# Kernel optimization log

Measured on AMD Instinct MI355X. Metric: run time of the kernel, lower is better.

## Reference

```python
import jax, jax.numpy as jnp
import numpy as np

D_MODEL, D_HEAD, N_HEADS, D_LATENT, D_ROPE = 2048, 128, 16, 512, 64
ROPE_BASE = 10000.0
SCALE = 1.0 / np.sqrt(D_HEAD + D_ROPE)


def _rope(x):
    # x: [B, H, T, d_rope]; GPT-NeoX style half-split rotary
    T, d = x.shape[-2], x.shape[-1]
    inv_freq = 1.0 / (ROPE_BASE ** (jnp.arange(0, d, 2, dtype=jnp.float32) / d))
    ang = jnp.arange(T, dtype=jnp.float32)[:, None] * inv_freq[None, :]  # [T, d/2]
    cos = jnp.concatenate([jnp.cos(ang), jnp.cos(ang)], axis=-1)  # [T, d]
    sin = jnp.concatenate([jnp.sin(ang), jnp.sin(ang)], axis=-1)
    x1, x2 = x[..., : d // 2], x[..., d // 2 :]
    rot = jnp.concatenate([-x2, x1], axis=-1)
    return x * cos + rot * sin


def setup_inputs() -> dict:
    key = jax.random.key(0)
    ks = jax.random.split(key, 8)
    B, T = 2, 2048
    s = 0.02
    inp = {
        "x": jax.random.normal(ks[0], (B, T, D_MODEL), jnp.float32),
        "w_q": jax.random.normal(ks[1], (D_MODEL, D_MODEL), jnp.float32) * s,
        "w_dkv": jax.random.normal(ks[2], (D_LATENT, D_MODEL), jnp.float32) * s,
        "w_ukv": jax.random.normal(ks[3], (2 * D_MODEL, D_LATENT), jnp.float32) * s,
        "w_o": jax.random.normal(ks[4], (D_MODEL, D_MODEL), jnp.float32) * s,
        "w_q_rot": jax.random.normal(ks[5], (N_HEADS * D_ROPE, D_MODEL), jnp.float32) * s,
        "w_k_rot": jax.random.normal(ks[6], (D_ROPE, D_MODEL), jnp.float32) * s,
        "mask": jnp.triu(jnp.ones((T, T), dtype=bool), 1),  # True = blocked (causal)
    }
    return inp


def reference(x, w_q, w_dkv, w_ukv, w_o, w_q_rot, w_k_rot, mask):
    B, T, _ = x.shape
    # content queries  [B, H, T, d_head]
    q = (x @ w_q.T).reshape(B, T, N_HEADS, D_HEAD).transpose(0, 2, 1, 3)
    # latent KV compression -> expansion
    dkv = x @ w_dkv.T                       # [B, T, d_latent]
    ukv = (dkv @ w_ukv.T).reshape(B, T, N_HEADS, 2 * D_HEAD).transpose(0, 2, 1, 3)
    k, v = ukv[..., :D_HEAD], ukv[..., D_HEAD:]
    # decoupled rope parts
    q_rot = (x @ w_q_rot.T).reshape(B, T, N_HEADS, D_ROPE).transpose(0, 2, 1, 3)
    k_rot = jnp.broadcast_to((x @ w_k_rot.T)[:, None, :, :], (B, N_HEADS, T, D_ROPE))
    q = jnp.concatenate([q, _rope(q_rot)], axis=-1)   # [B, H, T, d_head+d_rope]
    k = jnp.concatenate([k, _rope(k_rot)], axis=-1)
    # SDPA with True-means-blocked mask
    scores = jnp.einsum("bhqd,bhkd->bhqk", q, k) * SCALE
    scores = jnp.where(mask, -jnp.inf, scores)
    attn = jax.nn.softmax(scores, axis=-1)
    out = jnp.einsum("bhqk,bhkd->bhqd", attn, v)      # [B, H, T, d_head]
    out = out.transpose(0, 2, 1, 3).reshape(B, T, D_MODEL)
    return out @ w_o.T
```

## Files before the change

kernel.cpp:

```cpp
#include <hip/hip_runtime.h>
#include <hip/hip_bf16.h>
#include <math.h>

#define T_SEQ 2048
#define QSTR  3648

typedef __bf16 bf16x8 __attribute__((ext_vector_type(8)));
typedef float  f32x4  __attribute__((ext_vector_type(4)));
typedef float  f32x16 __attribute__((ext_vector_type(16)));
typedef unsigned int u32x4 __attribute__((ext_vector_type(4)));

#define GLOAD_LDS16(g, l) __builtin_amdgcn_global_load_lds( \
    (const __attribute__((address_space(1))) void*)(g),      \
    (__attribute__((address_space(3))) void*)(l), 16, 0, 0)

#define VMCNT(n) asm volatile("s_waitcnt vmcnt(" #n ")" ::: "memory")

static __device__ __forceinline__ unsigned cvtpk_bf16(float a, float b)
{
    unsigned r;
    asm("v_cvt_pk_bf16_f32 %0, %1, %2" : "=v"(r) : "v"(a), "v"(b));
    return r;
}

__global__ __launch_bounds__(256) void cast_bf16(const float* __restrict__ src,
                                                 __bf16* __restrict__ dst, int n)
{
    int i = (blockIdx.x * 256 + threadIdx.x) * 8;
    if (i < n) {
        float4 a = *reinterpret_cast<const float4*>(src + i);
        float4 b = *reinterpret_cast<const float4*>(src + i + 4);
        bf16x8 f;
        f[0] = (__bf16)a.x; f[1] = (__bf16)a.y; f[2] = (__bf16)a.z; f[3] = (__bf16)a.w;
        f[4] = (__bf16)b.x; f[5] = (__bf16)b.y; f[6] = (__bf16)b.z; f[7] = (__bf16)b.w;
        *reinterpret_cast<bf16x8*>(dst + i) = f;
    }
}

__global__ __launch_bounds__(256) void rope_ip(__bf16* buf, int shift, int stride,
                                               int total)
{
    int gid = blockIdx.x * 256 + threadIdx.x;
    if (gid >= total) return;
    int row = gid >> shift;
    int rem = gid & ((1 << shift) - 1);
    int hb = rem >> 5, j = rem & 31;
    int t = row & (T_SEQ - 1);
    const float L2B = 0.4152410118609203f;
    float freq = exp2f(-L2B * (float)j);
    float sn, cs;
    __sincosf((float)t * freq, &sn, &cs);
    size_t base = (size_t)row * stride + hb * 64 + j;
    float v1 = (float)buf[base], v2 = (float)buf[base + 32];
    buf[base]      = (__bf16)(v1 * cs - v2 * sn);
    buf[base + 32] = (__bf16)(v2 * cs + v1 * sn);
}

__global__ __launch_bounds__(256) void prep_v(const __bf16* __restrict__ ukv,
                                              __bf16* __restrict__ vtt)
{
    __shared__ __align__(16) __bf16 Ls[64 * 136];
    const int tid = threadIdx.x;
    const int u = blockIdx.x, bh = blockIdx.y;
    const int b = bh >> 4, h = bh & 15;
    const size_t base = (size_t)b * T_SEQ + u * 64;
    #pragma unroll
    for (int p = 0; p < 4; p++) {
        int c = tid + 256 * p;
        int k = c >> 4, dv8 = (c & 15) * 8;
        *reinterpret_cast<bf16x8*>(Ls + k * 136 + dv8) =
            *reinterpret_cast<const bf16x8*>(ukv + (base + k) * 4096 + h * 256 + 128 + dv8);
    }
    __syncthreads();
    #pragma unroll
    for (int p = 0; p < 4; p++) {
        int c = tid + 256 * p;
        int dv = c >> 3, kb = c & 7;
        bf16x8 f;
        #pragma unroll
        for (int i = 0; i < 8; i++) f[i] = Ls[(kb * 8 + i) * 136 + dv];
        *reinterpret_cast<bf16x8*>(vtt + (((size_t)bh * 32 + u) * 128 + dv) * 64
                                   + ((kb ^ (dv & 7)) << 3)) = f;
    }
}

template <typename OutT>
__global__ __launch_bounds__(512) void gemm_bt_8ph(const __bf16* __restrict__ A,
                                                   int lda,
                                                   const __bf16* __restrict__ B,
                                                   OutT* __restrict__ C,
                                                   int M, int N, int K)
{
    __shared__ __align__(16) __bf16 S[2 * 24576];
    const int tid  = threadIdx.x;
    const int lane = tid & 63;
    const int w    = tid >> 6;
    const int l15  = lane & 15, quad = lane >> 4;
    const int wm = w >> 2, wn = w & 3;
    const int m0 = blockIdx.y * 128, n0 = blockIdx.x * 256;
    const int NT = K >> 6;

    f32x4 acc[4][4] = {};

    const int lrA = tid >> 3, segA = tid & 7;

    auto stageA = [&](int T1, int h) {
        int d = T1 & 1;
        int g = ((lrA >> 5) << 6) + h * 32 + (lrA & 31);
        GLOAD_LDS16(A + (size_t)(m0 + g) * lda + T1 * 64 + ((segA ^ (lrA & 7)) << 3),
                    S + d * 24576 + h * 4096 + tid * 8);
    };
    auto stageB = [&](int T1, int h) {
        int d = T1 & 1;
        #pragma unroll
        for (int i = 0; i < 2; i++) {
            int c = i * 512 + tid;
            int lr = c >> 3, seg = c & 7;
            int g = n0 + ((lr >> 5) << 6) + h * 32 + (lr & 31);
            if (g >= N) g = N - 1;
            GLOAD_LDS16(B + (size_t)g * K + T1 * 64 + ((seg ^ (lr & 7)) << 3),
                        S + d * 24576 + 8192 + h * 8192 + c * 8);
        }
    };

#define PHASE(d, mh, nh, STAGE, WAIT) do {                                     \
    const __bf16* Ah_ = S + (d) * 24576 + (mh) * 4096;                         \
    const __bf16* Bh_ = S + (d) * 24576 + 8192 + (nh) * 8192;                  \
    bf16x8 af[2][2], bfr[2][2];                                                \
    _Pragma("unroll")                                                          \
    for (int mr = 0; mr < 2; mr++) {                                           \
        int ar = wm * 32 + mr * 16 + l15;                                      \
        _Pragma("unroll")                                                      \
        for (int kk = 0; kk < 2; kk++)                                         \
            af[mr][kk] = *reinterpret_cast<const bf16x8*>(                     \
                Ah_ + ar * 64 + (((kk * 4 + quad) ^ (ar & 7)) << 3));          \
    }                                                                          \
    _Pragma("unroll")                                                          \
    for (int nr = 0; nr < 2; nr++) {                                           \
        int br = wn * 32 + nr * 16 + l15;                                      \
        _Pragma("unroll")                                                      \
        for (int kk = 0; kk < 2; kk++)                                         \
            bfr[nr][kk] = *reinterpret_cast<const bf16x8*>(                    \
                Bh_ + br * 64 + (((kk * 4 + quad) ^ (br & 7)) << 3));          \
    }                                                                          \
    STAGE;                                                                     \
    WAIT;                                                                      \
    __builtin_amdgcn_s_barrier();                                              \
    asm volatile("s_waitcnt lgkmcnt(0)" ::: "memory");                         \
    __builtin_amdgcn_sched_barrier(0);                                         \
    __builtin_amdgcn_s_setprio(1);                                             \
    _Pragma("unroll")                                                          \
    for (int mr = 0; mr < 2; mr++)                                             \
        _Pragma("unroll")                                                      \
        for (int nr = 0; nr < 2; nr++)                                         \
            _Pragma("unroll")                                                  \
            for (int kk = 0; kk < 2; kk++)                                     \
                acc[(mh) * 2 + mr][(nh) * 2 + nr] =                            \
                    __builtin_amdgcn_mfma_f32_16x16x32_bf16(                   \
                        af[mr][kk], bfr[nr][kk],                               \
                        acc[(mh) * 2 + mr][(nh) * 2 + nr], 0, 0, 0);           \
    __builtin_amdgcn_s_setprio(0);                                             \
} while (0)

    stageA(0, 0);
    stageB(0, 0);
    stageB(0, 1);
    stageA(0, 1);
    VMCNT(3);
    __builtin_amdgcn_s_barrier();

    for (int T = 0; T < NT - 1; T++) {
        const int d = T & 1;
        PHASE(d, 0, 0, stageA(T + 1, 0), VMCNT(2));
        PHASE(d, 0, 1, stageB(T + 1, 0), VMCNT(3));
        PHASE(d, 1, 0, stageB(T + 1, 1), (void)0);
        PHASE(d, 1, 1, stageA(T + 1, 1), VMCNT(3));
    }
    {
        const int d = (NT - 1) & 1;
        PHASE(d, 0, 0, (void)0, VMCNT(1));
        PHASE(d, 0, 1, (void)0, VMCNT(0));
        PHASE(d, 1, 0, (void)0, (void)0);
        PHASE(d, 1, 1, (void)0, (void)0);
    }
#undef PHASE

    #pragma unroll
    for (int ai = 0; ai < 4; ai++) {
        #pragma unroll
        for (int bj = 0; bj < 4; bj++) {
            int col = n0 + wn * 64 + bj * 16 + l15;
            if (col < N) {
                #pragma unroll
                for (int r = 0; r < 4; r++) {
                    size_t row = m0 + wm * 64 + ai * 16 + quad * 4 + r;
                    C[row * (size_t)N + col] = (OutT)acc[ai][bj][r];
                }
            }
        }
    }
}

__global__ __launch_bounds__(256, 2) void flash_mfma(
    const __bf16* __restrict__ qcat, const __bf16* __restrict__ ukv,
    const __bf16* __restrict__ vtt, __bf16* __restrict__ obuf)
{
    __shared__ __align__(16) __bf16 LDS[40960];

    const int tid  = threadIdx.x;
    const int w    = tid >> 6;
    const int lane = tid & 63;
    const int l31  = lane & 31;
    const int lh   = lane >> 5;
    const int l15  = lane & 15;
    const int quad = lane >> 4;
    const int gx = blockIdx.x, gy = blockIdx.y;
    int bh, qi;
    if (gy < 16) { bh = gy * 2;            qi = gx; }
    else         { bh = (gy - 16) * 2 + 1; qi = 15 - gx; }
    const int b = bh >> 4, h = bh & 15;
    const int q0 = qi * 128;
    const float SCALE = 0.07216878364870323f;
    const size_t urow = (size_t)b * T_SEQ;

    const int q = q0 + 32 * w + l31;
    bf16x8 qf[12];
    {
        const __bf16* qrow = qcat + (urow + q) * QSTR + h * 128;
        #pragma unroll
        for (int dk = 0; dk < 8; dk++)
            qf[dk] = *reinterpret_cast<const bf16x8*>(qrow + 16 * dk + 8 * lh);
        const __bf16* qrr = qcat + (urow + q) * QSTR + 2048 + h * 64;
        #pragma unroll
        for (int dk = 0; dk < 4; dk++)
            qf[8 + dk] = *reinterpret_cast<const bf16x8*>(qrr + 16 * dk + 8 * lh);
    }

    f32x16 o[4] = {};
    float m_i = -INFINITY, l_i = 0.f;

    const int nunits = 2 * qi + 2;

    auto stage = [&](int x) {
        const int d1 = x & 1;
        const size_t roff = urow + (size_t)64 * x;
        #pragma unroll
        for (int p = 0; p < 4; p++) {
            int c = tid + 256 * p;
            int row = c >> 4, seg = c & 15;
            GLOAD_LDS16(ukv + (roff + row) * 4096 + h * 256 + ((seg ^ (row & 7)) << 3),
                        LDS + d1 * 8192 + c * 8);
        }
        #pragma unroll
        for (int p = 0; p < 2; p++) {
            int c = tid + 256 * p;
            int row = c >> 3, seg = c & 7;
            GLOAD_LDS16(qcat + (roff + row) * QSTR + 3072 + ((seg ^ (row & 7)) << 3),
                        LDS + 16384 + d1 * 4096 + c * 8);
        }
        const __bf16* vsrc = vtt + ((size_t)bh * 32 + x) * 8192;
        #pragma unroll
        for (int p = 0; p < 4; p++) {
            int c = tid + 256 * p;
            GLOAD_LDS16(vsrc + c * 8, LDS + 24576 + d1 * 8192 + c * 8);
        }
    };

    stage(0);
    VMCNT(0);
    __builtin_amdgcn_s_barrier();

    for (int u = 0; u < nunits; u++) {
        if (u + 1 < nunits) { stage(u + 1); VMCNT(10); }
        else                { VMCNT(0); }
        __builtin_amdgcn_s_barrier();
        __builtin_amdgcn_sched_barrier(0);

        const int d1 = u & 1;
        const __bf16* KN = LDS + d1 * 8192;
        const __bf16* KR = LDS + 16384 + d1 * 4096;
        const __bf16* VT = LDS + 24576 + d1 * 8192;
        const int key = l31 & 7;

        f32x16 s2[2] = {};
        __builtin_amdgcn_s_setprio(1);
        #pragma unroll
        for (int t = 0; t < 2; t++) {
            const __bf16* kn = KN + (32 * t + l31) * 128;
            const __bf16* kr = KR + (32 * t + l31) * 64;
            #pragma unroll
            for (int dk = 0; dk < 8; dk++) {
                bf16x8 kf = *reinterpret_cast<const bf16x8*>(kn + (((2 * dk + lh) ^ key) << 3));
                s2[t] = __builtin_amdgcn_mfma_f32_32x32x16_bf16(kf, qf[dk], s2[t], 0, 0, 0);
            }
            #pragma unroll
            for (int dk = 0; dk < 4; dk++) {
                bf16x8 kf = *reinterpret_cast<const bf16x8*>(kr + (((2 * dk + lh) ^ key) << 3));
                s2[t] = __builtin_amdgcn_mfma_f32_32x32x16_bf16(kf, qf[8 + dk], s2[t], 0, 0, 0);
            }
        }
        __builtin_amdgcn_s_setprio(0);

        const int k0 = 64 * u;
        const bool domask = (u + 2 >= nunits);
        float rmax = -INFINITY;
        #pragma unroll
        for (int t = 0; t < 2; t++)
            #pragma unroll
            for (int g = 0; g < 16; g++) {
                float v = s2[t][g] * SCALE;
                if (domask) {
                    int kg = k0 + 32 * t + (g & 3) + 8 * (g >> 2) + 4 * lh;
                    if (kg > q) v = -INFINITY;
                }
                s2[t][g] = v;
                rmax = fmaxf(rmax, v);
            }
        rmax = fmaxf(rmax, __shfl_xor(rmax, 32, 64));
        const float mnew  = fmaxf(m_i, rmax);
        const float alpha = __expf(m_i - mnew);
        m_i = mnew;
        float part = 0.f;
        #pragma unroll
        for (int t = 0; t < 2; t++)
            #pragma unroll
            for (int g = 0; g < 16; g++) {
                float pv = __expf(s2[t][g] - mnew);
                s2[t][g] = pv;
                part += pv;
            }
        l_i = l_i * alpha + part;
        #pragma unroll
        for (int dt = 0; dt < 4; dt++) o[dt] *= alpha;

        __builtin_amdgcn_s_setprio(1);
        #pragma unroll
        for (int t = 0; t < 2; t++) {
            unsigned Ap[4], Bp[4];
            #pragma unroll
            for (int g = 0; g < 4; g++) {
                Ap[g] = cvtpk_bf16(s2[t][4 * g],     s2[t][4 * g + 1]);
                Bp[g] = cvtpk_bf16(s2[t][4 * g + 2], s2[t][4 * g + 3]);
            }
            #pragma unroll
            for (int sub = 0; sub < 2; sub++) {
                unsigned xA = lh ? Ap[2 * sub] : Ap[2 * sub + 1];
                unsigned xB = lh ? Bp[2 * sub] : Bp[2 * sub + 1];
                unsigned rA = __shfl_xor(xA, 32, 64);
                unsigned rB = __shfl_xor(xB, 32, 64);
                u32x4 uv;
                uv[0] = lh ? rA : Ap[2 * sub];
                uv[1] = lh ? rB : Bp[2 * sub];
                uv[2] = lh ? Ap[2 * sub + 1] : rA;
                uv[3] = lh ? Bp[2 * sub + 1] : rB;
                bf16x8 pf = __builtin_bit_cast(bf16x8, uv);
                const int s = 2 * t + sub;
                #pragma unroll
                for (int dt = 0; dt < 4; dt++) {
                    bf16x8 vf = *reinterpret_cast<const bf16x8*>(
                        VT + (32 * dt + l31) * 64 + (((2 * s + lh) ^ key) << 3));
                    o[dt] = __builtin_amdgcn_mfma_f32_32x32x16_bf16(vf, pf, o[dt], 0, 0, 0);
                }
            }
        }
        __builtin_amdgcn_s_setprio(0);

        __builtin_amdgcn_sched_barrier(0);
        __builtin_amdgcn_s_barrier();
    }

    const float linv = 1.0f / (l_i + __shfl_xor(l_i, 32, 64));
    float* Os = reinterpret_cast<float*>(LDS);
    #pragma unroll
    for (int dt = 0; dt < 4; dt++)
        #pragma unroll
        for (int g = 0; g < 16; g++) {
            int d = 32 * dt + (g & 3) + 8 * (g >> 2) + 4 * lh;
            Os[(32 * w + l31) * 132 + d] = o[dt][g] * linv;
        }
    asm volatile("s_waitcnt lgkmcnt(0)" ::: "memory");
    __builtin_amdgcn_sched_barrier(0);
    #pragma unroll
    for (int p = 0; p < 8; p++) {
        int row = 32 * w + 4 * p + quad;
        float4 a  = *reinterpret_cast<const float4*>(Os + row * 132 + 8 * l15);
        float4 c2 = *reinterpret_cast<const float4*>(Os + row * 132 + 8 * l15 + 4);
        bf16x8 f;
        f[0] = (__bf16)a.x;  f[1] = (__bf16)a.y;  f[2] = (__bf16)a.z;  f[3] = (__bf16)a.w;
        f[4] = (__bf16)c2.x; f[5] = (__bf16)c2.y; f[6] = (__bf16)c2.z; f[7] = (__bf16)c2.w;
        *reinterpret_cast<bf16x8*>(obuf + (urow + q0 + row) * 2048 + h * 128 + 8 * l15) = f;
    }
}

extern "C" void kernel_launch(void* const* d_in, const int* in_sizes, int n_in,
                              void* d_out, int out_size, void* d_ws, size_t ws_size,
                              hipStream_t stream)
{
    const float* x      = (const float*)d_in[0];
    const float* w_q    = (const float*)d_in[1];
    const float* w_dkv  = (const float*)d_in[2];
    const float* w_ukv  = (const float*)d_in[3];
    const float* w_o    = (const float*)d_in[4];
    const float* w_qrot = (const float*)d_in[5];
    const float* w_krot = (const float*)d_in[6];
    float* out = (float*)d_out;

    const size_t M = 4096;
    __bf16* ws   = (__bf16*)d_ws;
    __bf16* xb   = ws;
    __bf16* wcat = xb + M * 2048;
    __bf16* wqb  = wcat;
    __bf16* wqrb = wcat + (size_t)2048 * 2048;
    __bf16* wkrb = wqrb + (size_t)1024 * 2048;
    __bf16* wdkb = wkrb + (size_t)64 * 2048;
    __bf16* wukb = wcat + (size_t)QSTR * 2048;
    __bf16* wob  = wukb + (size_t)4096 * 512;
    __bf16* qcat = wob  + (size_t)2048 * 2048;
    __bf16* ukv  = qcat + M * QSTR;
    __bf16* ao   = ukv  + M * 4096;
    __bf16* vtt  = ao   + M * 2048;

    dim3 blk(256);
    cast_bf16<<<4096, blk, 0, stream>>>(x,      xb,   4096 * 2048);
    cast_bf16<<<2048, blk, 0, stream>>>(w_q,    wqb,  2048 * 2048);
    cast_bf16<<<1024, blk, 0, stream>>>(w_qrot, wqrb, 1024 * 2048);
    cast_bf16<<<64,   blk, 0, stream>>>(w_krot, wkrb, 64 * 2048);
    cast_bf16<<<512,  blk, 0, stream>>>(w_dkv,  wdkb, 512 * 2048);
    cast_bf16<<<1024, blk, 0, stream>>>(w_ukv,  wukb, 4096 * 512);
    cast_bf16<<<2048, blk, 0, stream>>>(w_o,    wob,  2048 * 2048);

    gemm_bt_8ph<__bf16><<<dim3(15, 32), dim3(512), 0, stream>>>(
        xb, 2048, wcat, qcat, 4096, QSTR, 2048);
    gemm_bt_8ph<__bf16><<<dim3(16, 32), dim3(512), 0, stream>>>(
        qcat + 3136, QSTR, wukb, ukv, 4096, 4096, 512);

    rope_ip<<<8192, blk, 0, stream>>>(qcat + 2048, 9, QSTR, 4096 * 512);
    rope_ip<<<512,  blk, 0, stream>>>(qcat + 3072, 5, QSTR, 4096 * 32);
    prep_v<<<dim3(32, 32), blk, 0, stream>>>(ukv, vtt);

    flash_mfma<<<dim3(16, 32), blk, 0, stream>>>(qcat, ukv, vtt, ao);

    gemm_bt_8ph<float><<<dim3(8, 32), dim3(512), 0, stream>>>(
        ao, 2048, wob, out, 4096, 2048, 2048);
}
```

Baseline: 394.6 us.

## Merge weight casts into one launch and use 256x256 GEMM tiles for projections

The seven separate fp32-to-bf16 cast launches become one kernel that picks its source and destination from a cumulative block-offset table. The two projection GEMMs move from 128x256 to 256x256 tiles using a new four-phase pipelined kernel with 128 KB of shared memory and 32 accumulators per thread. Larger tiles raise arithmetic intensity and halve global reloads of the weight operand. The cost is fewer blocks (240 and 256) on a GPU with many CUs, plus higher register and LDS pressure.

```diff
diff --git a/kernel.cpp b/kernel.cpp
--- a/kernel.cpp
+++ b/kernel.cpp
@@ -23,18 +23,28 @@
     return r;
 }
 
-__global__ __launch_bounds__(256) void cast_bf16(const float* __restrict__ src,
-                                                 __bf16* __restrict__ dst, int n)
-{
-    int i = (blockIdx.x * 256 + threadIdx.x) * 8;
-    if (i < n) {
-        float4 a = *reinterpret_cast<const float4*>(src + i);
-        float4 b = *reinterpret_cast<const float4*>(src + i + 4);
-        bf16x8 f;
-        f[0] = (__bf16)a.x; f[1] = (__bf16)a.y; f[2] = (__bf16)a.z; f[3] = (__bf16)a.w;
-        f[4] = (__bf16)b.x; f[5] = (__bf16)b.y; f[6] = (__bf16)b.z; f[7] = (__bf16)b.w;
-        *reinterpret_cast<bf16x8*>(dst + i) = f;
-    }
+struct CastArgs {
+    const float* s[7];
+    __bf16*      d[7];
+    unsigned     cum[8];
+};
+
+__global__ __launch_bounds__(256) void cast_all(CastArgs a)
+{
+    const unsigned blk = blockIdx.x;
+    int idx = 0;
+    #pragma unroll
+    for (int i = 1; i < 7; i++) if (blk >= a.cum[i]) idx = i;
+    const unsigned local = blk - a.cum[idx];
+    const float* src = a.s[idx];
+    __bf16* dst = a.d[idx];
+    const int i = (int)(local * 256 + threadIdx.x) * 8;
+    float4 va = *reinterpret_cast<const float4*>(src + i);
+    float4 vb = *reinterpret_cast<const float4*>(src + i + 4);
+    bf16x8 f;
+    f[0] = (__bf16)va.x; f[1] = (__bf16)va.y; f[2] = (__bf16)va.z; f[3] = (__bf16)va.w;
+    f[4] = (__bf16)vb.x; f[5] = (__bf16)vb.y; f[6] = (__bf16)vb.z; f[7] = (__bf16)vb.w;
+    *reinterpret_cast<bf16x8*>(dst + i) = f;
 }
 
 __global__ __launch_bounds__(256) void rope_ip(__bf16* buf, int shift, int stride,
@@ -81,6 +91,133 @@
         for (int i = 0; i < 8; i++) f[i] = Ls[(kb * 8 + i) * 136 + dv];
         *reinterpret_cast<bf16x8*>(vtt + (((size_t)bh * 32 + u) * 128 + dv) * 64
                                    + ((kb ^ (dv & 7)) << 3)) = f;
+    }
+}
+
+template <typename OutT>
+__global__ __launch_bounds__(512, 2) void gemm_bt_256(const __bf16* __restrict__ A,
+                                                      int lda,
+                                                      const __bf16* __restrict__ B,
+                                                      OutT* __restrict__ C,
+                                                      int M, int N, int K)
+{
+    __shared__ __align__(16) __bf16 S[2 * 32768];
+    const int tid  = threadIdx.x;
+    const int lane = tid & 63;
+    const int w    = tid >> 6;
+    const int l15  = lane & 15, quad = lane >> 4;
+    const int wm = w >> 2, wn = w & 3;
+    const int m0 = blockIdx.y * 256, n0 = blockIdx.x * 256;
+    const int NT = K >> 6;
+
+    f32x4 acc[8][4] = {};
+    bf16x8 af[4][2], bfr[2][2];
+
+    auto stageA = [&](int T1, int h) {
+        int d = T1 & 1;
+        #pragma unroll
+        for (int i = 0; i < 2; i++) {
+            int c = i * 512 + tid;
+            int lr = c >> 3, seg = c & 7;
+            int g = ((lr >> 6) << 7) + h * 64 + (lr & 63);
+            GLOAD_LDS16(A + (size_t)(m0 + g) * lda + T1 * 64 + ((seg ^ (lr & 7)) << 3),
+                        S + d * 32768 + h * 8192 + c * 8);
+        }
+    };
+    auto stageB = [&](int T1, int h) {
+        int d = T1 & 1;
+        #pragma unroll
+        for (int i = 0; i < 2; i++) {
+            int c = i * 512 + tid;
+            int lr = c >> 3, seg = c & 7;
+            int g = n0 + ((lr >> 5) << 6) + h * 32 + (lr & 31);
+            if (g >= N) g = N - 1;
+            GLOAD_LDS16(B + (size_t)g * K + T1 * 64 + ((seg ^ (lr & 7)) << 3),
+                        S + d * 32768 + 16384 + h * 8192 + c * 8);
+        }
+    };
+
+#define LOADA(d, mh) do {                                                      \
+    const __bf16* Ah_ = S + (d) * 32768 + (mh) * 8192;                         \
+    _Pragma("unroll")                                                          \
+    for (int mi = 0; mi < 4; mi++) {                                           \
+        int lr = wm * 64 + mi * 16 + l15;                                      \
+        _Pragma("unroll")                                                      \
+        for (int kk = 0; kk < 2; kk++)                                         \
+            af[mi][kk] = *reinterpret_cast<const bf16x8*>(                     \
+                Ah_ + lr * 64 + (((kk * 4 + quad) ^ (lr & 7)) << 3));          \
+    }                                                                          \
+} while (0)
+
+#define LOADB(d, nh) do {                                                      \
+    const __bf16* Bh_ = S + (d) * 32768 + 16384 + (nh) * 8192;                 \
+    _Pragma("unroll")                                                          \
+    for (int ni = 0; ni < 2; ni++) {                                           \
+        int lr = wn * 32 + ni * 16 + l15;                                      \
+        _Pragma("unroll")                                                      \
+        for (int kk = 0; kk < 2; kk++)                                         \
+            bfr[ni][kk] = *reinterpret_cast<const bf16x8*>(                    \
+                Bh_ + lr * 64 + (((kk * 4 + quad) ^ (lr & 7)) << 3));          \
+    }                                                                          \
+} while (0)
+
+#define SEAL() do {                                                            \
+    __builtin_amdgcn_s_barrier();                                              \
+    asm volatile("s_waitcnt lgkmcnt(0)" ::: "memory");                         \
+    __builtin_amdgcn_sched_barrier(0);                                         \
+} while (0)
+
+#define MMA(mh, nh) do {                                                       \
+    __builtin_amdgcn_s_setprio(1);                                             \
+    _Pragma("unroll")                                                          \
+    for (int mi = 0; mi < 4; mi++)                                             \
+        _Pragma("unroll")                                                      \
+        for (int ni = 0; ni < 2; ni++)                                         \
+            _Pragma("unroll")                                                  \
+            for (int kk = 0; kk < 2; kk++)                                     \
+                acc[(mh) * 4 + mi][(nh) * 2 + ni] =                            \
+                    __builtin_amdgcn_mfma_f32_16x16x32_bf16(                   \
+                        af[mi][kk], bfr[ni][kk],                               \
+                        acc[(mh) * 4 + mi][(nh) * 2 + ni], 0, 0, 0);           \
+    __builtin_amdgcn_s_setprio(0);                                             \
+} while (0)
+
+    stageA(0, 0); stageB(0, 0); stageB(0, 1); stageA(0, 1);
+    VMCNT(4);
+    __builtin_amdgcn_s_barrier();
+
+    for (int T = 0; T < NT - 1; T++) {
+        const int d = T & 1;
+        LOADA(d, 0); LOADB(d, 0); stageA(T + 1, 0); VMCNT(4); SEAL(); MMA(0, 0);
+        LOADB(d, 1);              stageB(T + 1, 0); VMCNT(4); SEAL(); MMA(0, 1);
+        LOADA(d, 1);              stageB(T + 1, 1);           SEAL(); MMA(1, 1);
+        LOADB(d, 0);              stageA(T + 1, 1); VMCNT(4); SEAL(); MMA(1, 0);
+    }
+    {
+        const int d = (NT - 1) & 1;
+        LOADA(d, 0); LOADB(d, 0); VMCNT(2); SEAL(); MMA(0, 0);
+        LOADB(d, 1);              VMCNT(0); SEAL(); MMA(0, 1);
+        LOADA(d, 1);                        SEAL(); MMA(1, 1);
+        LOADB(d, 0);                        SEAL(); MMA(1, 0);
+    }
+#undef LOADA
+#undef LOADB
+#undef SEAL
+#undef MMA
+
+    #pragma unroll
+    for (int ai = 0; ai < 8; ai++) {
+        #pragma unroll
+        for (int bj = 0; bj < 4; bj++) {
+            int col = n0 + wn * 64 + bj * 16 + l15;
+            if (col < N) {
+                #pragma unroll
+                for (int r = 0; r < 4; r++) {
+                    size_t row = m0 + wm * 128 + ai * 16 + quad * 4 + r;
+                    C[row * (size_t)N + col] = (OutT)acc[ai][bj][r];
+                }
+            }
+        }
     }
 }
 
@@ -421,17 +558,28 @@
     __bf16* vtt  = ao   + M * 2048;
 
     dim3 blk(256);
-    cast_bf16<<<4096, blk, 0, stream>>>(x,      xb,   4096 * 2048);
-    cast_bf16<<<2048, blk, 0, stream>>>(w_q,    wqb,  2048 * 2048);
-    cast_bf16<<<1024, blk, 0, stream>>>(w_qrot, wqrb, 1024 * 2048);
-    cast_bf16<<<64,   blk, 0, stream>>>(w_krot, wkrb, 64 * 2048);
-    cast_bf16<<<512,  blk, 0, stream>>>(w_dkv,  wdkb, 512 * 2048);
-    cast_bf16<<<1024, blk, 0, stream>>>(w_ukv,  wukb, 4096 * 512);
-    cast_bf16<<<2048, blk, 0, stream>>>(w_o,    wob,  2048 * 2048);
-
-    gemm_bt_8ph<__bf16><<<dim3(15, 32), dim3(512), 0, stream>>>(
+
+    CastArgs ca;
+    ca.s[0] = x;      ca.d[0] = xb;
+    ca.s[1] = w_q;    ca.d[1] = wqb;
+    ca.s[2] = w_qrot; ca.d[2] = wqrb;
+    ca.s[3] = w_krot; ca.d[3] = wkrb;
+    ca.s[4] = w_dkv;  ca.d[4] = wdkb;
+    ca.s[5] = w_ukv;  ca.d[5] = wukb;
+    ca.s[6] = w_o;    ca.d[6] = wob;
+    ca.cum[0] = 0;
+    ca.cum[1] = ca.cum[0] + 4096;
+    ca.cum[2] = ca.cum[1] + 2048;
+    ca.cum[3] = ca.cum[2] + 1024;
+    ca.cum[4] = ca.cum[3] + 64;
+    ca.cum[5] = ca.cum[4] + 512;
+    ca.cum[6] = ca.cum[5] + 1024;
+    ca.cum[7] = ca.cum[6] + 2048;
+    cast_all<<<ca.cum[7], blk, 0, stream>>>(ca);
+
+    gemm_bt_256<__bf16><<<dim3(15, 16), dim3(512), 0, stream>>>(
         xb, 2048, wcat, qcat, 4096, QSTR, 2048);
-    gemm_bt_8ph<__bf16><<<dim3(16, 32), dim3(512), 0, stream>>>(
+    gemm_bt_256<__bf16><<<dim3(16, 16), dim3(512), 0, stream>>>(
         qcat + 3136, QSTR, wukb, ukv, 4096, 4096, 512);
 
     rope_ip<<<8192, blk, 0, stream>>>(qcat + 2048, 9, QSTR, 4096 * 512);
```

New measurement: 370.0 us. 6.2% less time.
